# Kernel tuning notes

Measured on AMD Instinct MI355X. Metric: run time of the kernel, lower is better.

The kernel has to match this reference:

```python
import jax, jax.numpy as jnp
import numpy as np

N = 65536        # flattened ray-sample count
K = 8            # net_kernels (experts)
WID = 64         # net_width
D = 32           # feature dim (num_output_channels)
POS_DEG = 2
VIEW_DEG = 4
DIN = D + (3 + 2 * POS_DEG * 3) + (3 + 2 * VIEW_DEG * 3)  # 74


def posenc(x, deg):
    # coord.pos_enc with min_deg=0, max_deg=deg, append_identity=True
    scales = 2.0 ** jnp.arange(deg, dtype=x.dtype)            # [deg]
    xb = (x[..., None, :] * scales[:, None]).reshape(*x.shape[:-1], deg * x.shape[-1])
    four = jnp.sin(jnp.concatenate([xb, xb + 0.5 * jnp.pi], axis=-1))
    return jnp.concatenate([x, four], axis=-1)


def multi_dense(idx, x, kernel, bias):
    # per-sample expert gather + small matmul: x [N,din], kernel [K,din,dout]
    w = kernel[idx]                                           # [N,din,dout]
    return jnp.einsum('ni,nio->no', x, w) + bias[idx]


def _he_uniform(key, shape):
    fan_in = shape[-2]
    lim = np.sqrt(6.0 / fan_in).astype(np.float32)
    return jax.random.uniform(key, shape, jnp.float32, -lim, lim)


def setup_inputs() -> dict:
    key = jax.random.key(0)
    ks = jax.random.split(key, 8)
    idxs = jax.random.randint(ks[0], (N, 1), 0, K, dtype=jnp.int32)
    positions = jax.random.normal(ks[1], (N, 3), jnp.float32)
    viewdirs = jax.random.normal(ks[2], (N, 3), jnp.float32)
    viewdirs = viewdirs / jnp.linalg.norm(viewdirs, axis=-1, keepdims=True)
    features = jax.random.normal(ks[3], (N, D), jnp.float32)
    W0 = _he_uniform(ks[4], (K, DIN, WID))
    b0 = jnp.zeros((K, WID), jnp.float32)
    W1 = _he_uniform(ks[5], (K, WID, WID))
    b1 = jnp.zeros((K, WID), jnp.float32)
    W2 = _he_uniform(ks[6], (K, WID, D))
    b2 = jnp.zeros((K, D), jnp.float32)
    return {'idxs': idxs, 'positions': positions, 'viewdirs': viewdirs,
            'features': features, 'W0': W0, 'b0': b0, 'W1': W1, 'b1': b1,
            'W2': W2, 'b2': b2}


def reference(idxs, positions, viewdirs, features, W0, b0, W1, b1, W2, b2):
    idx = idxs.reshape(-1)                                    # [N]
    x = jnp.concatenate([features,
                         posenc(positions, POS_DEG),
                         posenc(viewdirs, VIEW_DEG)], axis=-1)  # [N, DIN]
    h = jax.nn.relu(multi_dense(idx, x, W0, b0))              # [N, WID]
    h = jax.nn.relu(multi_dense(idx, h, W1, b1))              # [N, WID]
    return multi_dense(idx, h, W2, b2)                        # [N, D]
```

## Files before the change

kernel.cpp:

```cpp
#include <hip/hip_runtime.h>
#include <hip/hip_bf16.h>

#define NS    65536
#define KEXP  8
#define WID   64
#define DOUT  32
#define DIN   74
#define TM    64
#define XS    104
#define HS    72
#define GX    64
#define SEGCAP 65536

typedef __attribute__((ext_vector_type(8))) short short8;
typedef __attribute__((ext_vector_type(4))) float floatx4;

__device__ __forceinline__ unsigned short f2b(float f) {
  unsigned u = __builtin_bit_cast(unsigned, f);
  u = u + 0x7FFFu + ((u >> 16) & 1u);
  return (unsigned short)(u >> 16);
}


__global__ __launch_bounds__(256) void k_scatter(const int* __restrict__ idxs,
                                                 int* __restrict__ cursors,
                                                 unsigned short* __restrict__ bucket) {
  __shared__ int lc[KEXP];
  __shared__ int lbase[KEXP];
  const int tid = threadIdx.x;
  if (tid < KEXP) lc[tid] = 0;
  __syncthreads();
  const int gid = blockIdx.x * 256 + tid;
  const int e = idxs[gid];
  const int rank = atomicAdd(&lc[e], 1);
  __syncthreads();
  if (tid < KEXP) lbase[tid] = atomicAdd(&cursors[tid], lc[tid]);
  __syncthreads();
  bucket[(e << 16) + lbase[e] + rank] = (unsigned short)gid;
}

__global__ __launch_bounds__(256) void k_mlp(
    const int* __restrict__ cursors,
    const unsigned short* __restrict__ bucket,
    const float* __restrict__ pos,
    const float* __restrict__ view,
    const float* __restrict__ feat,
    const float* __restrict__ W0,
    const float* __restrict__ B0,
    const float* __restrict__ W1,
    const float* __restrict__ B1,
    const float* __restrict__ W2,
    const float* __restrict__ B2,
    float* __restrict__ out)
{
  const int e = blockIdx.y;
  const int segCnt = cursors[e];
  if ((int)blockIdx.x * TM >= segCnt) return;
  const int segStart = e << 16;
  const int tid = threadIdx.x;

  __shared__ __align__(16) unsigned short Xs[TM * XS];
  __shared__ __align__(16) unsigned short W0t[WID * XS];
  __shared__ __align__(16) unsigned short W1t[WID * HS];
  __shared__ __align__(16) unsigned short W2t[DOUT * HS];
  __shared__ __align__(16) unsigned short Hs[TM * HS];
  __shared__ float sb0[WID];
  __shared__ float sb1[WID];
  __shared__ float sb2[DOUT];
  __shared__ int sid[TM];

  for (int i = tid; i < TM * XS; i += 256) Xs[i] = 0;
  for (int i = tid; i < WID * XS; i += 256) W0t[i] = 0;
  __syncthreads();

  {
    const float* g0 = W0 + (size_t)e * DIN * WID;
    for (int g = tid; g < 19 * WID; g += 256) {
      const int o = g & 63, i4 = g >> 6, ib = i4 * 4;
      unsigned v0 = 0, v1 = 0;
      #pragma unroll
      for (int j = 0; j < 4; ++j) {
        const int i = ib + j;
        unsigned short w = (i < DIN) ? f2b(g0[i * WID + o]) : (unsigned short)0;
        if (j < 2) v0 |= (unsigned)w << (16 * j);
        else       v1 |= (unsigned)w << (16 * (j - 2));
      }
      *(uint2*)&W0t[o * XS + ib] = make_uint2(v0, v1);
    }
    const float* g1 = W1 + (size_t)e * WID * WID;
    for (int g = tid; g < 16 * WID; g += 256) {
      const int o = g & 63, i4 = g >> 6, ib = i4 * 4;
      unsigned v0, v1;
      v0 = (unsigned)f2b(g1[(ib + 0) * WID + o]) | ((unsigned)f2b(g1[(ib + 1) * WID + o]) << 16);
      v1 = (unsigned)f2b(g1[(ib + 2) * WID + o]) | ((unsigned)f2b(g1[(ib + 3) * WID + o]) << 16);
      *(uint2*)&W1t[o * HS + ib] = make_uint2(v0, v1);
    }
    const float* g2 = W2 + (size_t)e * WID * DOUT;
    for (int g = tid; g < 16 * DOUT; g += 256) {
      const int o = g & 31, i4 = g >> 5, ib = i4 * 4;
      unsigned v0, v1;
      v0 = (unsigned)f2b(g2[(ib + 0) * DOUT + o]) | ((unsigned)f2b(g2[(ib + 1) * DOUT + o]) << 16);
      v1 = (unsigned)f2b(g2[(ib + 2) * DOUT + o]) | ((unsigned)f2b(g2[(ib + 3) * DOUT + o]) << 16);
      *(uint2*)&W2t[o * HS + ib] = make_uint2(v0, v1);
    }
    if (tid < WID) {
      sb0[tid] = B0[e * WID + tid];
      sb1[tid] = B1[e * WID + tid];
    } else if (tid < WID + DOUT) {
      const int t = tid - WID;
      sb2[t] = B2[e * DOUT + t];
    }
  }
  __syncthreads();

  const int lane = tid & 63;
  const int wv = tid >> 6;
  const int quad = lane >> 4;
  const int r16 = lane & 15;
  const int rb = wv * 16;

  for (int tile = blockIdx.x; tile * TM < segCnt; tile += GX) {
    const int t0 = tile * TM;
    const int rows = min(TM, segCnt - t0);

    __syncthreads();

    const int r = lane;
    if (r < rows) {
      const int s = (int)bucket[segStart + t0 + r];
      unsigned short* xr = &Xs[r * XS];
      if (wv == 0) {
        sid[r] = s;
        const float4* fs = (const float4*)(feat + (size_t)s * DOUT);
        #pragma unroll
        for (int q = 0; q < 4; ++q) {
          float4 f = fs[q];
          xr[q * 4 + 0] = f2b(f.x);
          xr[q * 4 + 1] = f2b(f.y);
          xr[q * 4 + 2] = f2b(f.z);
          xr[q * 4 + 3] = f2b(f.w);
        }
      } else if (wv == 1) {
        const float4* fs = (const float4*)(feat + (size_t)s * DOUT);
        #pragma unroll
        for (int q = 4; q < 8; ++q) {
          float4 f = fs[q];
          xr[q * 4 + 0] = f2b(f.x);
          xr[q * 4 + 1] = f2b(f.y);
          xr[q * 4 + 2] = f2b(f.z);
          xr[q * 4 + 3] = f2b(f.w);
        }
      } else if (wv == 2) {
        float p[3];
        p[0] = pos[s * 3 + 0];
        p[1] = pos[s * 3 + 1];
        p[2] = pos[s * 3 + 2];
        #pragma unroll
        for (int d = 0; d < 3; ++d) xr[32 + d] = f2b(p[d]);
        #pragma unroll
        for (int si = 0; si < 2; ++si) {
          const float sc = (float)(1 << si);
          #pragma unroll
          for (int d = 0; d < 3; ++d) {
            const float a = p[d] * sc;
            xr[35 + si * 3 + d] = f2b(__sinf(a));
            xr[41 + si * 3 + d] = f2b(__cosf(a));
          }
        }
      } else {
        float v[3];
        v[0] = view[s * 3 + 0];
        v[1] = view[s * 3 + 1];
        v[2] = view[s * 3 + 2];
        #pragma unroll
        for (int d = 0; d < 3; ++d) xr[47 + d] = f2b(v[d]);
        #pragma unroll
        for (int si = 0; si < 4; ++si) {
          const float sc = (float)(1 << si);
          #pragma unroll
          for (int d = 0; d < 3; ++d) {
            const float a = v[d] * sc;
            xr[50 + si * 3 + d] = f2b(__sinf(a));
            xr[62 + si * 3 + d] = f2b(__cosf(a));
          }
        }
      }
    }
    __syncthreads();

    {
      const short8 a0 = *(const short8*)&Xs[(rb + r16) * XS + 0 + quad * 8];
      const short8 a1 = *(const short8*)&Xs[(rb + r16) * XS + 32 + quad * 8];
      const short8 a2 = *(const short8*)&Xs[(rb + r16) * XS + 64 + quad * 8];
      #pragma unroll
      for (int c = 0; c < 4; ++c) {
        const int n0 = c * 16;
        floatx4 acc = {0.f, 0.f, 0.f, 0.f};
        acc = __builtin_amdgcn_mfma_f32_16x16x32_bf16(
            a0, *(const short8*)&W0t[(n0 + r16) * XS + 0 + quad * 8], acc, 0, 0, 0);
        acc = __builtin_amdgcn_mfma_f32_16x16x32_bf16(
            a1, *(const short8*)&W0t[(n0 + r16) * XS + 32 + quad * 8], acc, 0, 0, 0);
        acc = __builtin_amdgcn_mfma_f32_16x16x32_bf16(
            a2, *(const short8*)&W0t[(n0 + r16) * XS + 64 + quad * 8], acc, 0, 0, 0);
        const float bias = sb0[n0 + r16];
        #pragma unroll
        for (int g = 0; g < 4; ++g) {
          const float vv = fmaxf(acc[g] + bias, 0.f);
          Hs[(rb + quad * 4 + g) * HS + n0 + r16] = f2b(vv);
        }
      }
    }

    {
      const short8 h0 = *(const short8*)&Hs[(rb + r16) * HS + 0 + quad * 8];
      const short8 h1 = *(const short8*)&Hs[(rb + r16) * HS + 32 + quad * 8];
      #pragma unroll
      for (int c = 0; c < 4; ++c) {
        const int n0 = c * 16;
        floatx4 acc = {0.f, 0.f, 0.f, 0.f};
        acc = __builtin_amdgcn_mfma_f32_16x16x32_bf16(
            h0, *(const short8*)&W1t[(n0 + r16) * HS + 0 + quad * 8], acc, 0, 0, 0);
        acc = __builtin_amdgcn_mfma_f32_16x16x32_bf16(
            h1, *(const short8*)&W1t[(n0 + r16) * HS + 32 + quad * 8], acc, 0, 0, 0);
        const float bias = sb1[n0 + r16];
        #pragma unroll
        for (int g = 0; g < 4; ++g) {
          const float vv = fmaxf(acc[g] + bias, 0.f);
          Hs[(rb + quad * 4 + g) * HS + n0 + r16] = f2b(vv);
        }
      }
    }

    {
      const short8 q0 = *(const short8*)&Hs[(rb + r16) * HS + 0 + quad * 8];
      const short8 q1 = *(const short8*)&Hs[(rb + r16) * HS + 32 + quad * 8];
      #pragma unroll
      for (int c = 0; c < 2; ++c) {
        const int n0 = c * 16;
        floatx4 acc = {0.f, 0.f, 0.f, 0.f};
        acc = __builtin_amdgcn_mfma_f32_16x16x32_bf16(
            q0, *(const short8*)&W2t[(n0 + r16) * HS + 0 + quad * 8], acc, 0, 0, 0);
        acc = __builtin_amdgcn_mfma_f32_16x16x32_bf16(
            q1, *(const short8*)&W2t[(n0 + r16) * HS + 32 + quad * 8], acc, 0, 0, 0);
        const float bias = sb2[n0 + r16];
        const int col = n0 + r16;
        #pragma unroll
        for (int g = 0; g < 4; ++g) {
          const int row = rb + quad * 4 + g;
          if (row < rows) {
            out[(size_t)sid[row] * DOUT + col] = acc[g] + bias;
          }
        }
      }
    }
  }
}

extern "C" void kernel_launch(void* const* d_in, const int* in_sizes, int n_in,
                              void* d_out, int out_size, void* d_ws, size_t ws_size,
                              hipStream_t stream) {
  const int* idxs        = (const int*)d_in[0];
  const float* pos       = (const float*)d_in[1];
  const float* view      = (const float*)d_in[2];
  const float* feat      = (const float*)d_in[3];
  const float* W0        = (const float*)d_in[4];
  const float* b0        = (const float*)d_in[5];
  const float* W1        = (const float*)d_in[6];
  const float* b1        = (const float*)d_in[7];
  const float* W2        = (const float*)d_in[8];
  const float* b2        = (const float*)d_in[9];
  float* out             = (float*)d_out;
  unsigned short* bucket = (unsigned short*)d_ws;
  int* cursors           = (int*)((char*)d_ws + (size_t)KEXP * SEGCAP * 2);

  hipMemsetAsync(cursors, 0, KEXP * sizeof(int), stream);
  k_scatter<<<NS / 256, 256, 0, stream>>>(idxs, cursors, bucket);
  dim3 grid(GX, KEXP);
  k_mlp<<<grid, 256, 0, stream>>>(cursors, bucket, pos, view, feat,
                                  W0, b0, W1, b1, W2, b2, out);
}
```

Before: 104.0 us.

## Replace global atomic cursors with per-block histograms and in-kernel prefix scan

Removes the memset and global atomics by having each scatter block write tokens into its own fixed 256-slot sub-bucket and a per-block expert histogram. Each MLP block then does a shared-memory Hillis-Steele scan over 256 block counts and binary-searches the prefix array to map a row index to its sub-bucket entry. This drops a memset launch and the cross-block atomic contention, at the cost of a redundant scan in every MLP block and a per-row binary search.

```diff
diff --git a/kernel.cpp b/kernel.cpp
--- a/kernel.cpp
+++ b/kernel.cpp
@@ -10,7 +10,7 @@
 #define XS    104
 #define HS    72
 #define GX    64
-#define SEGCAP 65536
+#define NB    256
 
 typedef __attribute__((ext_vector_type(8))) short short8;
 typedef __attribute__((ext_vector_type(4))) float floatx4;
@@ -23,24 +23,23 @@
 
 
 __global__ __launch_bounds__(256) void k_scatter(const int* __restrict__ idxs,
-                                                 int* __restrict__ cursors,
-                                                 unsigned short* __restrict__ bucket) {
+                                                 unsigned short* __restrict__ bucket,
+                                                 int* __restrict__ hist) {
   __shared__ int lc[KEXP];
-  __shared__ int lbase[KEXP];
   const int tid = threadIdx.x;
+  const int b = blockIdx.x;
   if (tid < KEXP) lc[tid] = 0;
   __syncthreads();
-  const int gid = blockIdx.x * 256 + tid;
+  const int gid = b * 256 + tid;
   const int e = idxs[gid];
   const int rank = atomicAdd(&lc[e], 1);
-  __syncthreads();
-  if (tid < KEXP) lbase[tid] = atomicAdd(&cursors[tid], lc[tid]);
-  __syncthreads();
-  bucket[(e << 16) + lbase[e] + rank] = (unsigned short)gid;
+  bucket[(e << 16) + (b << 8) + rank] = (unsigned short)gid;
+  __syncthreads();
+  if (tid < KEXP) hist[b * KEXP + tid] = lc[tid];
 }
 
 __global__ __launch_bounds__(256) void k_mlp(
-    const int* __restrict__ cursors,
+    const int* __restrict__ hist,
     const unsigned short* __restrict__ bucket,
     const float* __restrict__ pos,
     const float* __restrict__ view,
@@ -54,9 +53,6 @@
     float* __restrict__ out)
 {
   const int e = blockIdx.y;
-  const int segCnt = cursors[e];
-  if ((int)blockIdx.x * TM >= segCnt) return;
-  const int segStart = e << 16;
   const int tid = threadIdx.x;
 
   __shared__ __align__(16) unsigned short Xs[TM * XS];
@@ -68,6 +64,21 @@
   __shared__ float sb1[WID];
   __shared__ float sb2[DOUT];
   __shared__ int sid[TM];
+  __shared__ unsigned cn[NB];
+  __shared__ unsigned pref[NB];
+
+  cn[tid] = (unsigned)hist[tid * KEXP + e];
+  pref[tid] = cn[tid];
+  __syncthreads();
+  #pragma unroll
+  for (int st = 1; st < NB; st <<= 1) {
+    const unsigned v = (tid >= st) ? pref[tid - st] : 0u;
+    __syncthreads();
+    pref[tid] += v;
+    __syncthreads();
+  }
+  const int segCnt = (int)pref[NB - 1];
+  if ((int)blockIdx.x * TM >= segCnt) return;
 
   for (int i = tid; i < TM * XS; i += 256) Xs[i] = 0;
   for (int i = tid; i < WID * XS; i += 256) W0t[i] = 0;
@@ -127,7 +138,16 @@
 
     const int r = lane;
     if (r < rows) {
-      const int s = (int)bucket[segStart + t0 + r];
+      const int p = t0 + r;
+      int lo = 0, hi = NB - 1;
+      #pragma unroll
+      for (int it = 0; it < 8; ++it) {
+        const int mid = (lo + hi) >> 1;
+        if (pref[mid] > (unsigned)p) hi = mid; else lo = mid + 1;
+      }
+      const int sb_ = lo;
+      const int local = p - (int)(pref[sb_] - cn[sb_]);
+      const int s = (int)bucket[(e << 16) + (sb_ << 8) + local];
       unsigned short* xr = &Xs[r * XS];
       if (wv == 0) {
         sid[r] = s;
@@ -151,35 +171,35 @@
           xr[q * 4 + 3] = f2b(f.w);
         }
       } else if (wv == 2) {
-        float p[3];
-        p[0] = pos[s * 3 + 0];
-        p[1] = pos[s * 3 + 1];
-        p[2] = pos[s * 3 + 2];
-        #pragma unroll
-        for (int d = 0; d < 3; ++d) xr[32 + d] = f2b(p[d]);
+        float p3[3];
+        p3[0] = pos[s * 3 + 0];
+        p3[1] = pos[s * 3 + 1];
+        p3[2] = pos[s * 3 + 2];
+        #pragma unroll
+        for (int d = 0; d < 3; ++d) xr[32 + d] = f2b(p3[d]);
         #pragma unroll
         for (int si = 0; si < 2; ++si) {
           const float sc = (float)(1 << si);
           #pragma unroll
           for (int d = 0; d < 3; ++d) {
-            const float a = p[d] * sc;
+            const float a = p3[d] * sc;
             xr[35 + si * 3 + d] = f2b(__sinf(a));
             xr[41 + si * 3 + d] = f2b(__cosf(a));
           }
         }
       } else {
-        float v[3];
-        v[0] = view[s * 3 + 0];
-        v[1] = view[s * 3 + 1];
-        v[2] = view[s * 3 + 2];
-        #pragma unroll
-        for (int d = 0; d < 3; ++d) xr[47 + d] = f2b(v[d]);
+        float v3[3];
+        v3[0] = view[s * 3 + 0];
+        v3[1] = view[s * 3 + 1];
+        v3[2] = view[s * 3 + 2];
+        #pragma unroll
+        for (int d = 0; d < 3; ++d) xr[47 + d] = f2b(v3[d]);
         #pragma unroll
         for (int si = 0; si < 4; ++si) {
           const float sc = (float)(1 << si);
           #pragma unroll
           for (int d = 0; d < 3; ++d) {
-            const float a = v[d] * sc;
+            const float a = v3[d] * sc;
             xr[50 + si * 3 + d] = f2b(__sinf(a));
             xr[62 + si * 3 + d] = f2b(__cosf(a));
           }
@@ -271,11 +291,10 @@
   const float* b2        = (const float*)d_in[9];
   float* out             = (float*)d_out;
   unsigned short* bucket = (unsigned short*)d_ws;
-  int* cursors           = (int*)((char*)d_ws + (size_t)KEXP * SEGCAP * 2);
-
-  hipMemsetAsync(cursors, 0, KEXP * sizeof(int), stream);
-  k_scatter<<<NS / 256, 256, 0, stream>>>(idxs, cursors, bucket);
+  int* hist              = (int*)((char*)d_ws + (size_t)KEXP * NB * 256 * 2);
+
+  k_scatter<<<NB, 256, 0, stream>>>(idxs, bucket, hist);
   dim3 grid(GX, KEXP);
-  k_mlp<<<grid, 256, 0, stream>>>(cursors, bucket, pos, view, feat,
+  k_mlp<<<grid, 256, 0, stream>>>(hist, bucket, pos, view, feat,
                                   W0, b0, W1, b1, W2, b2, out);
 }
```

Result: no change. 102.7 us (-1.3%).
